# Kernel optimization log

Measured on AMD Instinct MI355X. Metric: run time of the kernel, lower is better.

Reference implementation:

```python
import jax, jax.numpy as jnp
import numpy as np
import math

B, T, D = 2, 2048, 2048
H, DH = 16, 128
DKV, DQ, DR = 512, 1024, 64
ROPE_BASE = 500000.0
EPS = 1e-6
SCALE = 1.0 / math.sqrt(DH + DR)


def setup_inputs() -> dict:
    key = jax.random.key(0)
    ks = jax.random.split(key, 12)
    s = 0.02
    return {
        'x': jax.random.normal(ks[0], (B, T, D), jnp.float32),
        'W_DQ': jax.random.normal(ks[1], (D, DQ), jnp.float32) * s,
        'W_UQ': jax.random.normal(ks[2], (DQ, H * DH), jnp.float32) * s,
        'W_QR': jax.random.normal(ks[3], (DQ, H * DR), jnp.float32) * s,
        'W_DKV': jax.random.normal(ks[4], (D, DKV), jnp.float32) * s,
        'W_UK': jax.random.normal(ks[5], (DKV, H * DH), jnp.float32) * s,
        'W_UV': jax.random.normal(ks[6], (DKV, H * DH), jnp.float32) * s,
        'W_KR': jax.random.normal(ks[7], (D, DR), jnp.float32) * s,
        'W_O': jax.random.normal(ks[8], (H * DH, D), jnp.float32) * s,
        'q_norm_w': jnp.ones((DQ,), jnp.float32),
        'kv_norm_w': jnp.ones((DKV,), jnp.float32),
    }


def _rmsnorm(v, w):
    n = jax.lax.rsqrt(jnp.mean(v * v, axis=-1, keepdims=True) + EPS)
    return v * n * w


def _rotate_half(v):
    v1, v2 = jnp.split(v, 2, axis=-1)
    return jnp.concatenate([-v2, v1], axis=-1)


def _rope_tables(seq_len):
    inv_freq = 1.0 / (ROPE_BASE ** (jnp.arange(0, DR, 2, dtype=jnp.float32) / DR))
    t = jnp.arange(seq_len, dtype=jnp.float32)
    freqs = jnp.outer(t, inv_freq)              # (S, DR/2)
    emb = jnp.concatenate([freqs, freqs], -1)   # (S, DR)
    return jnp.cos(emb), jnp.sin(emb)


def reference(x, W_DQ, W_UQ, W_QR, W_DKV, W_UK, W_UV, W_KR, W_O, q_norm_w, kv_norm_w):
    # Query path: low-rank compress -> RMSNorm -> up-project (content + rope parts)
    c_Q = _rmsnorm(x @ W_DQ, q_norm_w)                               # (B,T,DQ)
    q_C = (c_Q @ W_UQ).reshape(B, T, H, DH).transpose(0, 2, 1, 3)    # (B,H,T,DH)
    q_R = (c_Q @ W_QR).reshape(B, T, H, DR).transpose(0, 2, 1, 3)    # (B,H,T,DR)
    # KV path: joint low-rank latent + decoupled rope key
    c_KV = _rmsnorm(x @ W_DKV, kv_norm_w)                            # (B,T,DKV)
    k_C = (c_KV @ W_UK).reshape(B, T, H, DH).transpose(0, 2, 1, 3)   # (B,H,T,DH)
    v_C = (c_KV @ W_UV).reshape(B, T, H, DH).transpose(0, 2, 1, 3)   # (B,H,T,DH)
    k_R = (x @ W_KR)[:, None, :, :]                                  # (B,1,T,DR) shared across heads
    # Decoupled RoPE
    cos, sin = _rope_tables(T)
    cos = cos[None, None]; sin = sin[None, None]                     # (1,1,T,DR)
    q_R = q_R * cos + _rotate_half(q_R) * sin
    k_R = k_R * cos + _rotate_half(k_R) * sin
    k_R = jnp.broadcast_to(k_R, (B, H, T, DR))
    q = jnp.concatenate([q_C, q_R], axis=-1)                         # (B,H,T,DH+DR)
    k = jnp.concatenate([k_C, k_R], axis=-1)
    # Causal attention with MLA scale 1/sqrt(d_head + d_rope)
    scores = jnp.einsum('bhqd,bhkd->bhqk', q, k) * SCALE
    causal = jnp.tril(jnp.ones((T, T), bool))
    scores = jnp.where(causal, scores, jnp.finfo(scores.dtype).min)
    attn = jax.nn.softmax(scores, axis=-1)
    out = jnp.einsum('bhqk,bhkd->bhqd', attn, v_C)                   # (B,H,T,DH)
    out = out.transpose(0, 2, 1, 3).reshape(B, T, H * DH)
    return out @ W_O                                                 # (B,T,D)
```

## Files before the change

kernel.cpp:

```cpp
#include <hip/hip_runtime.h>
#include <cstdint>
#include <cstddef>

#define B_   2
#define T_   2048
#define D_   2048
#define H_   16
#define DH_  128
#define DQ_  1024
#define DKV_ 512
#define DR_  64
#define M_   4096
#define SCALE_ 0.07216878364870323f
#define SC2_   0.10412808709930322f
#define LN_BASE_ 13.122363377404328f

typedef unsigned short u16;
typedef __attribute__((ext_vector_type(8))) short short8;
typedef __attribute__((ext_vector_type(4))) float f32x4;

__device__ __forceinline__ float b2f(u16 u) { return __uint_as_float(((uint32_t)u) << 16); }
__device__ __forceinline__ u16 f2b(float f) {
    uint32_t x = __float_as_uint(f);
    return (u16)((x + 0x7fffu + ((x >> 16) & 1u)) >> 16);
}
__device__ __forceinline__ u16 f2b_fast(float f) {
    return (u16)((__float_as_uint(f) + 0x8000u) >> 16);
}

__device__ __forceinline__ void gload_lds16(const u16* src, u16* dst) {
    __builtin_amdgcn_global_load_lds(
        (const __attribute__((address_space(1))) uint32_t*)(uintptr_t)src,
        (__attribute__((address_space(3))) uint32_t*)(uintptr_t)dst, 16, 0, 0);
}

struct TPack {
    const float* src[8];
    u16*         dst[8];
    int K[8];
    int N[8];
    int ntx[8];
    int start[9];
};

__global__ __launch_bounds__(256) void prep_k(TPack p, const float* __restrict__ x,
                                              u16* __restrict__ xb, int ntr) {
    const int bid = blockIdx.x;
    if (bid < ntr) {
        __shared__ float tile[32][33];
        int w = 0;
#pragma unroll
        for (int i = 1; i < 8; ++i) if (bid >= p.start[i]) w = i;
        const int lt = bid - p.start[w];
        const int bx = lt % p.ntx[w], by = lt / p.ntx[w];
        const float* in = p.src[w];
        u16* out = p.dst[w];
        const int K = p.K[w], N = p.N[w];
        const int k0 = by * 32, n0 = bx * 32;
        const int tx = threadIdx.x & 31, ty = threadIdx.x >> 5;
#pragma unroll
        for (int i = 0; i < 4; ++i) {
            int k = k0 + ty + i * 8;
            int n = n0 + tx;
            tile[ty + i * 8][tx] = (n < N) ? in[(size_t)k * N + n] : 0.f;
        }
        __syncthreads();
#pragma unroll
        for (int i = 0; i < 4; ++i) {
            int n = n0 + ty + i * 8;
            out[(size_t)n * K + k0 + tx] = f2b(tile[tx][ty + i * 8]);
        }
    } else {
        const int i = ((bid - ntr) * 256 + threadIdx.x) * 4;
        const float4 v = *(const float4*)(x + i);
        ushort4 o;
        o.x = f2b(v.x); o.y = f2b(v.y); o.z = f2b(v.z); o.w = f2b(v.w);
        *(ushort4*)(xb + i) = o;
    }
}

template <int OUT_BF16>
__global__ __launch_bounds__(256) void gemm_tn(const u16* __restrict__ A,
                                               const u16* __restrict__ Bt,
                                               void* __restrict__ Cv,
                                               int N, int K) {
    __shared__ __attribute__((aligned(16))) u16 lA[128 * 32];
    __shared__ __attribute__((aligned(16))) u16 lB[128 * 32];
    const int m0 = blockIdx.y * 128, n0 = blockIdx.x * 128;
    const int tid = threadIdx.x, wave = tid >> 6, lane = tid & 63;
    const int wm = (wave >> 1) * 64, wn = (wave & 1) * 64;
    const int r = lane & 15, kq = lane >> 4;

    f32x4 acc[4][4];
#pragma unroll
    for (int i = 0; i < 4; ++i)
#pragma unroll
        for (int j = 0; j < 4; ++j) acc[i][j] = (f32x4){0.f, 0.f, 0.f, 0.f};

    for (int kk = 0; kk < K; kk += 32) {
#pragma unroll
        for (int p = 0; p < 2; ++p) {
            const int c = p * 256 + wave * 64 + lane;
            const u16* ga = A  + (size_t)(m0 + (c >> 2)) * K + kk + (c & 3) * 8;
            const u16* gb = Bt + (size_t)(n0 + (c >> 2)) * K + kk + (c & 3) * 8;
            u16* la = lA + (size_t)(p * 256 + wave * 64) * 8;
            u16* lb = lB + (size_t)(p * 256 + wave * 64) * 8;
            gload_lds16(ga, la);
            gload_lds16(gb, lb);
        }
        __syncthreads();
        short8 av[4], bv[4];
#pragma unroll
        for (int mi = 0; mi < 4; ++mi)
            av[mi] = *(const short8*)&lA[(wm + mi * 16 + r) * 32 + kq * 8];
#pragma unroll
        for (int ni = 0; ni < 4; ++ni)
            bv[ni] = *(const short8*)&lB[(wn + ni * 16 + r) * 32 + kq * 8];
#pragma unroll
        for (int mi = 0; mi < 4; ++mi)
#pragma unroll
            for (int ni = 0; ni < 4; ++ni)
                acc[mi][ni] = __builtin_amdgcn_mfma_f32_16x16x32_bf16(
                    av[mi], bv[ni], acc[mi][ni], 0, 0, 0);
        __syncthreads();
    }
    const int r4 = (lane >> 4) * 4, cc = lane & 15;
#pragma unroll
    for (int mi = 0; mi < 4; ++mi)
#pragma unroll
        for (int ni = 0; ni < 4; ++ni)
#pragma unroll
            for (int i = 0; i < 4; ++i) {
                const int row = m0 + wm + mi * 16 + r4 + i;
                const int col = n0 + wn + ni * 16 + cc;
                const float v = acc[mi][ni][i];
                if (OUT_BF16) ((u16*)Cv)[(size_t)row * N + col] = f2b(v);
                else          ((float*)Cv)[(size_t)row * N + col] = v;
            }
}

#define S_BM 256
#define S_BN 256
#define S_BK 64

__device__ __forceinline__ void gemm256_core(
    const u16* __restrict__ A, const u16* __restrict__ Bt, int K,
    int m0, int n0, int tid, f32x4 (&acc)[8][4],
    u16 (*sA)[S_BM * S_BK], u16 (*sB)[S_BN * S_BK]) {
    const int lane = tid & 63;
    const int wave = tid >> 6;
    const int wm = wave >> 2;
    const int r = lane & 15, kq = lane >> 4;
    const int wn = wave & 3;

    const u16* gA[4]; const u16* gB[4]; int dOf[4];
#pragma unroll
    for (int is = 0; is < 4; ++is) {
        const int c = is * 512 + tid;
        const int row = c >> 3, c16 = c & 7;
        gA[is] = A  + (size_t)(m0 + row) * K + ((c16 ^ (row & 7)) * 8);
        gB[is] = Bt + (size_t)(n0 + row) * K + ((c16 ^ (row & 7)) * 8);
        dOf[is] = c * 8;
    }

    const int NKT = K >> 6;

    auto STG = [&](int arr, int half, int bs, int kk) {
        u16* dst = arr ? (u16*)sB[bs] : (u16*)sA[bs];
        const u16** g = arr ? gB : gA;
#pragma unroll
        for (int is = half * 2; is < half * 2 + 2; ++is)
            gload_lds16(g[is] + kk, dst + dOf[is]);
    };

    STG(0, 0, 0, 0); STG(0, 1, 0, 0); STG(1, 0, 0, 0); STG(1, 1, 0, 0);

    short8 af[4][2], bf[2][2];
    for (int kt = 0; kt < NKT; ++kt) {
        const int cur = kt & 1;
        const int kk = (kt + 1) * 64;
        const int pf = (kt + 1 < NKT);
        const u16* cA = sA[cur];
        const u16* cB = sB[cur];

        auto lda = [&](int row, int g) -> short8 {
            return *(const short8*)&cA[row * 64 + ((g ^ (row & 7)) * 8)];
        };
        auto ldb = [&](int row, int g) -> short8 {
            return *(const short8*)&cB[row * 64 + ((g ^ (row & 7)) * 8)];
        };

#pragma unroll
        for (int ph = 0; ph < 4; ++ph) {
            const int mh = ph >> 1;
            const int nh = (ph == 1 || ph == 2) ? 1 : 0;
            if (pf) STG(ph >> 1, ph & 1, cur ^ 1, kk);
            if (ph == 0) {
                if (pf) asm volatile("s_waitcnt vmcnt(2)" ::: "memory");
                else    asm volatile("s_waitcnt vmcnt(0)" ::: "memory");
            }
            __builtin_amdgcn_s_barrier();
            asm volatile("" ::: "memory");
            if (!(ph & 1)) {
#pragma unroll
                for (int mi = 0; mi < 4; ++mi)
#pragma unroll
                    for (int ks = 0; ks < 2; ++ks)
                        af[mi][ks] = lda(wm * 128 + mh * 64 + mi * 16 + r, ks * 4 + kq);
            }
#pragma unroll
            for (int ni = 0; ni < 2; ++ni)
#pragma unroll
                for (int ks = 0; ks < 2; ++ks)
                    bf[ni][ks] = ldb(wn * 64 + nh * 32 + ni * 16 + r, ks * 4 + kq);
#pragma unroll
            for (int ks = 0; ks < 2; ++ks)
#pragma unroll
                for (int mi = 0; mi < 4; ++mi)
#pragma unroll
                    for (int ni = 0; ni < 2; ++ni)
                        acc[mh * 4 + mi][nh * 2 + ni] =
                            __builtin_amdgcn_mfma_f32_16x16x32_bf16(
                                af[mi][ks], bf[ni][ks],
                                acc[mh * 4 + mi][nh * 2 + ni], 0, 0, 0);
            asm volatile("" ::: "memory");
            __builtin_amdgcn_s_barrier();
            asm volatile("" ::: "memory");
        }
    }
}

__global__ __launch_bounds__(512, 1) void gemm256p_k(
    const u16* __restrict__ A0, const u16* __restrict__ B0,
    u16* __restrict__ C0, int N0c, int K0,
    const u16* __restrict__ A1, const u16* __restrict__ B1,
    u16* __restrict__ C1, int N1c, int K1,
    u16* __restrict__ Vt, int vcol0, int nx0)
{
    __shared__ __attribute__((aligned(16))) u16 sA[2][S_BM * S_BK];
    __shared__ __attribute__((aligned(16))) u16 sB[2][S_BN * S_BK];
    const int sel = (int)blockIdx.x >= nx0;
    const u16* A  = sel ? A1 : A0;
    const u16* Bt = sel ? B1 : B0;
    const int  K  = sel ? K1 : K0;
    const int lbx = sel ? (blockIdx.x - nx0) : blockIdx.x;
    const int m0 = blockIdx.y * S_BM, n0 = lbx * S_BN;
    const int tid = threadIdx.x, lane = tid & 63;
    const int wave = tid >> 6, wm = wave >> 2, wn = wave & 3;
    const int kq = lane >> 4;

    f32x4 acc[8][4];
#pragma unroll
    for (int i = 0; i < 8; ++i)
#pragma unroll
        for (int j = 0; j < 4; ++j) acc[i][j] = (f32x4){0.f, 0.f, 0.f, 0.f};

    gemm256_core(A, Bt, K, m0, n0, tid, acc, sA, sB);

    const int r4c = kq * 4, cc = lane & 15;
    if (!sel) {
#pragma unroll
        for (int mf = 0; mf < 8; ++mf)
#pragma unroll
            for (int nf = 0; nf < 4; ++nf)
#pragma unroll
                for (int i = 0; i < 4; ++i) {
                    const int row = m0 + wm * 128 + mf * 16 + r4c + i;
                    const int col = n0 + wn * 64 + nf * 16 + cc;
                    C0[(size_t)row * N0c + col] = f2b(acc[mf][nf][i]);
                }
    } else if (n0 < vcol0) {
#pragma unroll
        for (int mf = 0; mf < 8; ++mf)
#pragma unroll
            for (int nf = 0; nf < 4; ++nf)
#pragma unroll
                for (int i = 0; i < 4; ++i) {
                    const int row = m0 + wm * 128 + mf * 16 + r4c + i;
                    const int col = n0 + wn * 64 + nf * 16 + cc;
                    C1[(size_t)row * N1c + col] = f2b(acc[mf][nf][i]);
                }
    } else {
#pragma unroll
        for (int mf = 0; mf < 8; ++mf)
#pragma unroll
            for (int nf = 0; nf < 4; ++nf) {
                const int tp = m0 + wm * 128 + mf * 16 + r4c;
                const int c  = n0 - vcol0 + wn * 64 + nf * 16 + cc;
                u16 tmp[4];
#pragma unroll
                for (int i = 0; i < 4; ++i) tmp[i] = f2b(acc[mf][nf][i]);
                *(ushort4*)&Vt[((size_t)((tp >> 11) * 2048 + c)) * 2048 + (tp & 2047)]
                    = *(ushort4*)tmp;
            }
    }
}

__global__ __launch_bounds__(512, 1) void gemm256o_k(
    const u16* __restrict__ A, const u16* __restrict__ Bt,
    float* __restrict__ Cf, int N, int K)
{
    __shared__ __attribute__((aligned(16))) u16 sA[2][S_BM * S_BK];
    __shared__ __attribute__((aligned(16))) u16 sB[2][S_BN * S_BK];
    const int m0 = blockIdx.y * S_BM, n0 = blockIdx.x * S_BN;
    const int tid = threadIdx.x, lane = tid & 63;
    const int wave = tid >> 6, wm = wave >> 2, wn = wave & 3;
    const int kq = lane >> 4;

    f32x4 acc[8][4];
#pragma unroll
    for (int i = 0; i < 8; ++i)
#pragma unroll
        for (int j = 0; j < 4; ++j) acc[i][j] = (f32x4){0.f, 0.f, 0.f, 0.f};

    gemm256_core(A, Bt, K, m0, n0, tid, acc, sA, sB);

    const int r4c = kq * 4, cc = lane & 15;
#pragma unroll
    for (int mf = 0; mf < 8; ++mf)
#pragma unroll
        for (int nf = 0; nf < 4; ++nf)
#pragma unroll
            for (int i = 0; i < 4; ++i) {
                const int row = m0 + wm * 128 + mf * 16 + r4c + i;
                const int col = n0 + wn * 64 + nf * 16 + cc;
                Cf[(size_t)row * N + col] = acc[mf][nf][i];
            }
}

__global__ __launch_bounds__(256) void normrope_k(const u16* __restrict__ P1,
                                                  const float* __restrict__ qnw,
                                                  const float* __restrict__ kvnw,
                                                  u16* __restrict__ cQb,
                                                  u16* __restrict__ cKVb,
                                                  u16* __restrict__ kRb) {
    const int which = blockIdx.y;
    if (which < 2) {
        const int row = blockIdx.x;
        const int N = which ? 512 : 1024;
        const int off = which ? 1024 : 0;
        const float* w = which ? kvnw : qnw;
        u16* outp = which ? cKVb : cQb;
        const u16* src = P1 + (size_t)row * 1664 + off;
        const int j = threadIdx.x * 4;
        float v[4] = {0.f, 0.f, 0.f, 0.f};
        if (j < N) {
            ushort4 u = *(const ushort4*)(src + j);
            v[0] = b2f(u.x); v[1] = b2f(u.y); v[2] = b2f(u.z); v[3] = b2f(u.w);
        }
        float ss = v[0]*v[0] + v[1]*v[1] + v[2]*v[2] + v[3]*v[3];
#pragma unroll
        for (int offc = 32; offc; offc >>= 1) ss += __shfl_down(ss, offc);
        __shared__ float red[4];
        const int wave = threadIdx.x >> 6, lane = threadIdx.x & 63;
        if (lane == 0) red[wave] = ss;
        __syncthreads();
        const float tot = red[0] + red[1] + red[2] + red[3];
        const float sc = rsqrtf(tot / (float)N + 1e-6f);
        if (j < N) {
            ushort4 o;
            o.x = f2b(v[0] * sc * w[j]);
            o.y = f2b(v[1] * sc * w[j + 1]);
            o.z = f2b(v[2] * sc * w[j + 2]);
            o.w = f2b(v[3] * sc * w[j + 3]);
            *(ushort4*)(outp + (size_t)row * N + j) = o;
        }
    } else {
        if (blockIdx.x >= 1024) return;
        const int row = blockIdx.x * 4 + (threadIdx.x >> 6);
        const int j = threadIdx.x & 63;
        const int t = row & (T_ - 1);
        const int i = j & 31;
        const float invf = __expf(-LN_BASE_ * (float)(2 * i) * (1.0f / 64.0f));
        const float ang = (float)t * invf;
        const float c = cosf(ang), s = sinf(ang);
        const u16* src = P1 + (size_t)row * 1664 + 1536;
        const float v = b2f(src[j]);
        const float rot = (j < 32) ? -b2f(src[j + 32]) : b2f(src[j - 32]);
        kRb[(size_t)row * 64 + j] = f2b(v * c + rot * s);
    }
}

#define ABQ  128
#define ABK  64
#define NW   8
#define KSTR 200
#define VSTR 72
#define PSTR 72
#define VOFF 12800
#define KVSZ 22016
#define QSTRIDE 3072
#define KSTRIDE 4096

__global__ __launch_bounds__(512, 1) void attn_mfma_k(
    const u16* __restrict__ qC,
    const u16* __restrict__ kC, const u16* __restrict__ kR,
    const u16* __restrict__ Vt, u16* __restrict__ outp)
{
    __shared__ __attribute__((aligned(16))) u16 sKV[3][KVSZ];
    __shared__ __attribute__((aligned(16))) u16 sP[NW * 16 * PSTR];

    const int h = blockIdx.x, b = blockIdx.z;
    const int qb = b ? (15 - (int)blockIdx.y) : (int)blockIdx.y;
    const int q0 = qb * ABQ;
    const int tid = threadIdx.x, wave = tid >> 6, lane = tid & 63;
    const int r = lane & 15, kq = lane >> 4, r4 = kq * 4;
    const int wq = wave * 16;

    const u16* gsrc[6]; int gstep[6]; int doff[6];
#pragma unroll
    for (int j = 0; j < 6; ++j) {
        const int i = wave + NW * j;
        const int slot = (i < 43) ? i : (i - 43);
        if (slot < 25) {
            const int s = slot * 64 + lane;
            const int rr2 = s / 25;
            int cc = s - rr2 * 25;
            if (cc > 23) cc = 0;
            if (cc < 16) {
                gsrc[j] = kC + (size_t)(b * T_ + rr2) * KSTRIDE + h * 128 + cc * 8;
                gstep[j] = ABK * KSTRIDE;
            } else {
                gsrc[j] = kR + (size_t)(b * T_ + rr2) * 64 + (cc - 16) * 8;
                gstep[j] = ABK * 64;
            }
            doff[j] = slot * 512;
        } else {
            const int sl = slot - 25;
            const int s = sl * 64 + lane;
            const int rr2 = s / 9;
            int cc = s - rr2 * 9;
            if (cc > 7) cc = 0;
            gsrc[j] = Vt + ((size_t)(b * H_ + h) * 128 + rr2) * T_ + cc * 8;
            gstep[j] = ABK;
            doff[j] = VOFF + sl * 512;
        }
    }

    short8 qf[6];
    {
        const int t = q0 + wq + r;
        const u16* qcrow = qC + (size_t)(b * T_ + t) * QSTRIDE + h * 128 + kq * 8;
#pragma unroll
        for (int kc = 0; kc < 4; ++kc) qf[kc] = *(const short8*)(qcrow + kc * 32);
        const u16* qrraw = qC + (size_t)(b * T_ + t) * QSTRIDE + 2048 + h * 64 + kq * 8;
        const short8 q0v = *(const short8*)(qrraw);
        const short8 q1v = *(const short8*)(qrraw + 32);
        short8 o0, o1;
#pragma unroll
        for (int j = 0; j < 8; ++j) {
            const int i = kq * 8 + j;
            const float invf = __expf(-LN_BASE_ * (float)(2 * i) * (1.0f / 64.0f));
            const float ang = (float)t * invf;
            const float cs = cosf(ang), sn = sinf(ang);
            const float a = b2f((u16)q0v[j]), bb = b2f((u16)q1v[j]);
            o0[j] = (short)f2b(a * cs - bb * sn);
            o1[j] = (short)f2b(bb * cs + a * sn);
        }
        qf[4] = o0; qf[5] = o1;
    }

    f32x4 Oa[8];
#pragma unroll
    for (int nt = 0; nt < 8; ++nt) Oa[nt] = (f32x4){0.f, 0.f, 0.f, 0.f};
    float Lrow[4] = {0.f, 0.f, 0.f, 0.f};

    u16* myP = sP + wave * 16 * PSTR;

    auto STAGE = [&](int kt2, int bs) {
        u16* dst = &sKV[bs][0];
#pragma unroll
        for (int j = 0; j < 6; ++j)
            gload_lds16(gsrc[j] + (size_t)kt2 * (size_t)gstep[j], dst + doff[j]);
    };

    const int nkt = 2 * qb + 2;
    STAGE(0, 0);
    STAGE(1, 1);
    for (int kt = 0; kt < nkt; ++kt) {
        const int cur = kt % 3;
        if (kt == 0 || kt >= nkt - 1) {
            asm volatile("s_waitcnt vmcnt(0)" ::: "memory");
        } else {
            asm volatile("s_waitcnt vmcnt(6)" ::: "memory");
        }
        __builtin_amdgcn_s_barrier();
        asm volatile("" ::: "memory");

        const u16* cK = &sKV[cur][0];
        const u16* cV = &sKV[cur][VOFF];
        const int k0 = kt * ABK;

        f32x4 Sa[4];
#pragma unroll
        for (int nt = 0; nt < 4; ++nt) Sa[nt] = (f32x4){0.f, 0.f, 0.f, 0.f};
#pragma unroll
        for (int kc = 0; kc < 6; ++kc) {
            short8 kf[4];
#pragma unroll
            for (int nt = 0; nt < 4; ++nt)
                kf[nt] = *(const short8*)&cK[(nt * 16 + r) * KSTR + (kc * 4 + kq) * 8];
#pragma unroll
            for (int nt = 0; nt < 4; ++nt)
                Sa[nt] = __builtin_amdgcn_mfma_f32_16x16x32_bf16(
                    qf[kc], kf[nt], Sa[nt], 0, 0, 0);
        }

        if (kt < nkt - 2) {
#pragma unroll
            for (int i = 0; i < 4; ++i) {
                float sm = 0.f;
#pragma unroll
                for (int nt = 0; nt < 4; ++nt) {
                    const float p = exp2f(Sa[nt][i] * SC2_);
                    sm += p;
                    myP[(r4 + i) * PSTR + nt * 16 + r] = f2b_fast(p);
                }
                Lrow[i] += sm;
            }
        } else {
#pragma unroll
            for (int i = 0; i < 4; ++i) {
                const int grow = q0 + wq + r4 + i;
                float sm = 0.f;
#pragma unroll
                for (int nt = 0; nt < 4; ++nt) {
                    float p = exp2f(Sa[nt][i] * SC2_);
                    p = (k0 + nt * 16 + r > grow) ? 0.f : p;
                    sm += p;
                    myP[(r4 + i) * PSTR + nt * 16 + r] = f2b_fast(p);
                }
                Lrow[i] += sm;
            }
        }

#pragma unroll
        for (int kc2 = 0; kc2 < 2; ++kc2) {
            const short8 pf = *(const short8*)&myP[r * PSTR + (kc2 * 4 + kq) * 8];
#pragma unroll
            for (int nt = 0; nt < 8; ++nt) {
                const short8 vf = *(const short8*)&cV[(nt * 16 + r) * VSTR + (kc2 * 4 + kq) * 8];
                Oa[nt] = __builtin_amdgcn_mfma_f32_16x16x32_bf16(
                    pf, vf, Oa[nt], 0, 0, 0);
            }
        }

        if (kt + 2 < nkt) STAGE(kt + 2, (kt + 2) % 3);
    }

#pragma unroll
    for (int i = 0; i < 4; ++i) {
        float L = Lrow[i];
        L += __shfl_xor(L, 1);
        L += __shfl_xor(L, 2);
        L += __shfl_xor(L, 4);
        L += __shfl_xor(L, 8);
        const float inv = 1.0f / L;
        const int t = q0 + wq + r4 + i;
        u16* orow = outp + (size_t)(b * T_ + t) * 2048 + h * 128;
#pragma unroll
        for (int nt = 0; nt < 8; ++nt)
            orow[nt * 16 + r] = f2b(Oa[nt][i] * inv);
    }
}

extern "C" void kernel_launch(void* const* d_in, const int* in_sizes, int n_in,
                              void* d_out, int out_size, void* d_ws, size_t ws_size,
                              hipStream_t stream) {
    (void)in_sizes; (void)n_in; (void)out_size; (void)ws_size;
    const float* x     = (const float*)d_in[0];
    const float* W_DQ  = (const float*)d_in[1];
    const float* W_UQ  = (const float*)d_in[2];
    const float* W_QR  = (const float*)d_in[3];
    const float* W_DKV = (const float*)d_in[4];
    const float* W_UK  = (const float*)d_in[5];
    const float* W_UV  = (const float*)d_in[6];
    const float* W_KR  = (const float*)d_in[7];
    const float* W_O   = (const float*)d_in[8];
    const float* qnw   = (const float*)d_in[9];
    const float* kvnw  = (const float*)d_in[10];
    float* out = (float*)d_out;

    char* base = (char*)d_ws;
    size_t o = 0;
    auto alloc = [&](size_t bytes) {
        char* r = base + o;
        o += (bytes + 255) & ~(size_t)255;
        return r;
    };
    u16* WT1  = (u16*)alloc((size_t)1664 * 2048 * 2);
    u16* WT2  = (u16*)alloc((size_t)3072 * 1024 * 2);
    u16* WT3  = (u16*)alloc((size_t)4096 * 512 * 2);
    u16* WT_O = (u16*)alloc((size_t)2048 * 2048 * 2);
    u16* xb   = (u16*)alloc((size_t)M_ * 2048 * 2);
    u16* U1   = (u16*)alloc((size_t)M_ * 2048 * 2);
    u16* P2   = (u16*)alloc((size_t)M_ * 3072 * 2);
    u16* P3   = (u16*)alloc((size_t)M_ * 4096 * 2);
    u16* cQb  = (u16*)alloc((size_t)M_ * 1024 * 2);
    u16* cKVb = (u16*)alloc((size_t)M_ * 512 * 2);
    u16* qRb  = (u16*)alloc((size_t)M_ * 1024 * 2);
    u16* kRb  = (u16*)alloc((size_t)M_ * 64 * 2);
    (void)qRb;
    u16* P1       = U1;
    u16* attn_out = U1;
    u16* Vt       = xb;

    TPack tp;
    const float* srcs[8] = {W_DQ, W_DKV, W_KR, W_UQ, W_QR, W_UK, W_UV, W_O};
    u16* dsts[8] = {WT1, WT1 + (size_t)1024*2048, WT1 + (size_t)1536*2048,
                    WT2, WT2 + (size_t)2048*1024,
                    WT3, WT3 + (size_t)2048*512, WT_O};
    const int Ks[8]   = {2048, 2048, 2048, 1024, 1024, 512, 512, 2048};
    const int Ns[8]   = {1024,  512,   64, 2048, 1024, 2048, 2048, 2048};
    const int ntxs[8] = {  32,   16,    4,   64,   32,   64,   64,   64};
    int cum = 0;
    for (int i = 0; i < 8; ++i) {
        tp.src[i] = srcs[i]; tp.dst[i] = dsts[i];
        tp.K[i] = Ks[i]; tp.N[i] = Ns[i]; tp.ntx[i] = ntxs[i];
        tp.start[i] = cum;
        cum += ntxs[i] * (Ks[i] / 32);
    }
    tp.start[8] = cum;
    const int ncast = (M_ * D_) / 1024;
    prep_k<<<cum + ncast, 256, 0, stream>>>(tp, x, xb, cum);

    gemm_tn<1><<<dim3(1664/128, M_/128), 256, 0, stream>>>(xb, WT1, (void*)P1, 1664, 2048);

    normrope_k<<<dim3(M_, 3), 256, 0, stream>>>(P1, qnw, kvnw, cQb, cKVb, kRb);

    gemm256p_k<<<dim3(3072/256 + 4096/256, M_/256), 512, 0, stream>>>(
        cQb,  WT2, P2, 3072, 1024,
        cKVb, WT3, P3, 4096, 512,
        Vt, 2048, 3072/256);

    attn_mfma_k<<<dim3(H_, T_/ABQ, B_), 512, 0, stream>>>(P2, P3, kRb, Vt, attn_out);

    gemm256o_k<<<dim3(2048/256, M_/256), 512, 0, stream>>>(attn_out, WT_O, out, 2048, 2048);
}
```

Baseline: 391.5 us.

## Enlarge attention query tile to 256 rows with double-buffered KV staging

```diff
diff --git a/kernel.cpp b/kernel.cpp
--- a/kernel.cpp
+++ b/kernel.cpp
@@ -294,38 +294,6 @@
                     = *(ushort4*)tmp;
             }
     }
-}
-
-__global__ __launch_bounds__(512, 1) void gemm256o_k(
-    const u16* __restrict__ A, const u16* __restrict__ Bt,
-    float* __restrict__ Cf, int N, int K)
-{
-    __shared__ __attribute__((aligned(16))) u16 sA[2][S_BM * S_BK];
-    __shared__ __attribute__((aligned(16))) u16 sB[2][S_BN * S_BK];
-    const int m0 = blockIdx.y * S_BM, n0 = blockIdx.x * S_BN;
-    const int tid = threadIdx.x, lane = tid & 63;
-    const int wave = tid >> 6, wm = wave >> 2, wn = wave & 3;
-    const int kq = lane >> 4;
-
-    f32x4 acc[8][4];
-#pragma unroll
-    for (int i = 0; i < 8; ++i)
-#pragma unroll
-        for (int j = 0; j < 4; ++j) acc[i][j] = (f32x4){0.f, 0.f, 0.f, 0.f};
-
-    gemm256_core(A, Bt, K, m0, n0, tid, acc, sA, sB);
-
-    const int r4c = kq * 4, cc = lane & 15;
-#pragma unroll
-    for (int mf = 0; mf < 8; ++mf)
-#pragma unroll
-        for (int nf = 0; nf < 4; ++nf)
-#pragma unroll
-            for (int i = 0; i < 4; ++i) {
-                const int row = m0 + wm * 128 + mf * 16 + r4c + i;
-                const int col = n0 + wn * 64 + nf * 16 + cc;
-                Cf[(size_t)row * N + col] = acc[mf][nf][i];
-            }
 }
 
 __global__ __launch_bounds__(256) void normrope_k(const u16* __restrict__ P1,
@@ -381,7 +349,7 @@
     }
 }
 
-#define ABQ  128
+#define ABQ  256
 #define ABK  64
 #define NW   8
 #define KSTR 200
@@ -397,15 +365,15 @@
     const u16* __restrict__ kC, const u16* __restrict__ kR,
     const u16* __restrict__ Vt, u16* __restrict__ outp)
 {
-    __shared__ __attribute__((aligned(16))) u16 sKV[3][KVSZ];
-    __shared__ __attribute__((aligned(16))) u16 sP[NW * 16 * PSTR];
+    __shared__ __attribute__((aligned(16))) u16 sKV[2][KVSZ];
+    __shared__ __attribute__((aligned(16))) u16 sP[NW * 32 * PSTR];
 
     const int h = blockIdx.x, b = blockIdx.z;
-    const int qb = b ? (15 - (int)blockIdx.y) : (int)blockIdx.y;
+    const int qb = b ? (7 - (int)blockIdx.y) : (int)blockIdx.y;
     const int q0 = qb * ABQ;
     const int tid = threadIdx.x, wave = tid >> 6, lane = tid & 63;
     const int r = lane & 15, kq = lane >> 4, r4 = kq * 4;
-    const int wq = wave * 16;
+    const int wq = wave * 32;
 
     const u16* gsrc[6]; int gstep[6]; int doff[6];
 #pragma unroll
@@ -437,12 +405,13 @@
         }
     }
 
-    short8 qf[6];
-    {
-        const int t = q0 + wq + r;
+    short8 qf[2][6];
+#pragma unroll
+    for (int mt = 0; mt < 2; ++mt) {
+        const int t = q0 + wq + mt * 16 + r;
         const u16* qcrow = qC + (size_t)(b * T_ + t) * QSTRIDE + h * 128 + kq * 8;
 #pragma unroll
-        for (int kc = 0; kc < 4; ++kc) qf[kc] = *(const short8*)(qcrow + kc * 32);
+        for (int kc = 0; kc < 4; ++kc) qf[mt][kc] = *(const short8*)(qcrow + kc * 32);
         const u16* qrraw = qC + (size_t)(b * T_ + t) * QSTRIDE + 2048 + h * 64 + kq * 8;
         const short8 q0v = *(const short8*)(qrraw);
         const short8 q1v = *(const short8*)(qrraw + 32);
@@ -457,15 +426,17 @@
             o0[j] = (short)f2b(a * cs - bb * sn);
             o1[j] = (short)f2b(bb * cs + a * sn);
         }
-        qf[4] = o0; qf[5] = o1;
-    }
-
-    f32x4 Oa[8];
-#pragma unroll
-    for (int nt = 0; nt < 8; ++nt) Oa[nt] = (f32x4){0.f, 0.f, 0.f, 0.f};
-    float Lrow[4] = {0.f, 0.f, 0.f, 0.f};
-
-    u16* myP = sP + wave * 16 * PSTR;
+        qf[mt][4] = o0; qf[mt][5] = o1;
+    }
+
+    f32x4 Oa[2][8];
+#pragma unroll
+    for (int mt = 0; mt < 2; ++mt)
+#pragma unroll
+        for (int nt = 0; nt < 8; ++nt) Oa[mt][nt] = (f32x4){0.f, 0.f, 0.f, 0.f};
+    float Lrow[2][4] = {{0.f,0.f,0.f,0.f},{0.f,0.f,0.f,0.f}};
+
+    u16* myP = sP + (size_t)wave * 32 * PSTR;
 
     auto STAGE = [&](int kt2, int bs) {
         u16* dst = &sKV[bs][0];
@@ -474,12 +445,12 @@
             gload_lds16(gsrc[j] + (size_t)kt2 * (size_t)gstep[j], dst + doff[j]);
     };
 
-    const int nkt = 2 * qb + 2;
+    const int nkt = 4 * qb + 4;
     STAGE(0, 0);
-    STAGE(1, 1);
     for (int kt = 0; kt < nkt; ++kt) {
-        const int cur = kt % 3;
-        if (kt == 0 || kt >= nkt - 1) {
+        const int cur = kt & 1;
+        if (kt + 1 < nkt) STAGE(kt + 1, cur ^ 1);
+        if (kt == 0 || kt + 1 >= nkt) {
             asm volatile("s_waitcnt vmcnt(0)" ::: "memory");
         } else {
             asm volatile("s_waitcnt vmcnt(6)" ::: "memory");
@@ -491,9 +462,11 @@
         const u16* cV = &sKV[cur][VOFF];
         const int k0 = kt * ABK;
 
-        f32x4 Sa[4];
-#pragma unroll
-        for (int nt = 0; nt < 4; ++nt) Sa[nt] = (f32x4){0.f, 0.f, 0.f, 0.f};
+        f32x4 Sa[2][4];
+#pragma unroll
+        for (int mt = 0; mt < 2; ++mt)
+#pragma unroll
+            for (int nt = 0; nt < 4; ++nt) Sa[mt][nt] = (f32x4){0.f, 0.f, 0.f, 0.f};
 #pragma unroll
         for (int kc = 0; kc < 6; ++kc) {
             short8 kf[4];
@@ -501,67 +474,82 @@
             for (int nt = 0; nt < 4; ++nt)
                 kf[nt] = *(const short8*)&cK[(nt * 16 + r) * KSTR + (kc * 4 + kq) * 8];
 #pragma unroll
-            for (int nt = 0; nt < 4; ++nt)
-                Sa[nt] = __builtin_amdgcn_mfma_f32_16x16x32_bf16(
-                    qf[kc], kf[nt], Sa[nt], 0, 0, 0);
-        }
-
-        if (kt < nkt - 2) {
-#pragma unroll
-            for (int i = 0; i < 4; ++i) {
-                float sm = 0.f;
-#pragma unroll
-                for (int nt = 0; nt < 4; ++nt) {
-                    const float p = exp2f(Sa[nt][i] * SC2_);
-                    sm += p;
-                    myP[(r4 + i) * PSTR + nt * 16 + r] = f2b_fast(p);
+            for (int mt = 0; mt < 2; ++mt)
+#pragma unroll
+                for (int nt = 0; nt < 4; ++nt)
+                    Sa[mt][nt] = __builtin_amdgcn_mfma_f32_16x16x32_bf16(
+                        qf[mt][kc], kf[nt], Sa[mt][nt], 0, 0, 0);
+        }
+
+        if (kt < nkt - 4) {
+#pragma unroll
+            for (int mt = 0; mt < 2; ++mt)
+#pragma unroll
+                for (int i = 0; i < 4; ++i) {
+                    float sm = 0.f;
+#pragma unroll
+                    for (int nt = 0; nt < 4; ++nt) {
+                        const float p = exp2f(Sa[mt][nt][i] * SC2_);
+                        sm += p;
+                        myP[(mt * 16 + r4 + i) * PSTR + nt * 16 + r] = f2b_fast(p);
+                    }
+                    Lrow[mt][i] += sm;
                 }
-                Lrow[i] += sm;
-            }
         } else {
 #pragma unroll
-            for (int i = 0; i < 4; ++i) {
-                const int grow = q0 + wq + r4 + i;
-                float sm = 0.f;
-#pragma unroll
-                for (int nt = 0; nt < 4; ++nt) {
-                    float p = exp2f(Sa[nt][i] * SC2_);
-                    p = (k0 + nt * 16 + r > grow) ? 0.f : p;
-                    sm += p;
-                    myP[(r4 + i) * PSTR + nt * 16 + r] = f2b_fast(p);
+            for (int mt = 0; mt < 2; ++mt)
+#pragma unroll
+                for (int i = 0; i < 4; ++i) {
+                    const int grow = q0 + wq + mt * 16 + r4 + i;
+                    float sm = 0.f;
+#pragma unroll
+                    for (int nt = 0; nt < 4; ++nt) {
+                        float p = exp2f(Sa[mt][nt][i] * SC2_);
+                        p = (k0 + nt * 16 + r > grow) ? 0.f : p;
+                        sm += p;
+                        myP[(mt * 16 + r4 + i) * PSTR + nt * 16 + r] = f2b_fast(p);
+                    }
+                    Lrow[mt][i] += sm;
                 }
-                Lrow[i] += sm;
-            }
         }
 
 #pragma unroll
         for (int kc2 = 0; kc2 < 2; ++kc2) {
-            const short8 pf = *(const short8*)&myP[r * PSTR + (kc2 * 4 + kq) * 8];
+            short8 pf[2];
+#pragma unroll
+            for (int mt = 0; mt < 2; ++mt)
+                pf[mt] = *(const short8*)&myP[(mt * 16 + r) * PSTR + (kc2 * 4 + kq) * 8];
 #pragma unroll
             for (int nt = 0; nt < 8; ++nt) {
                 const short8 vf = *(const short8*)&cV[(nt * 16 + r) * VSTR + (kc2 * 4 + kq) * 8];
-                Oa[nt] = __builtin_amdgcn_mfma_f32_16x16x32_bf16(
-                    pf, vf, Oa[nt], 0, 0, 0);
+#pragma unroll
+                for (int mt = 0; mt < 2; ++mt)
+                    Oa[mt][nt] = __builtin_amdgcn_mfma_f32_16x16x32_bf16(
+                        pf[mt], vf, Oa[mt][nt], 0, 0, 0);
             }
         }
 
-        if (kt + 2 < nkt) STAGE(kt + 2, (kt + 2) % 3);
-    }
-
-#pragma unroll
-    for (int i = 0; i < 4; ++i) {
-        float L = Lrow[i];
-        L += __shfl_xor(L, 1);
-        L += __shfl_xor(L, 2);
-        L += __shfl_xor(L, 4);
-        L += __shfl_xor(L, 8);
-        const float inv = 1.0f / L;
-        const int t = q0 + wq + r4 + i;
-        u16* orow = outp + (size_t)(b * T_ + t) * 2048 + h * 128;
-#pragma unroll
-        for (int nt = 0; nt < 8; ++nt)
-            orow[nt * 16 + r] = f2b(Oa[nt][i] * inv);
-    }
+        asm volatile("" ::: "memory");
+        __builtin_amdgcn_s_barrier();
+        asm volatile("" ::: "memory");
+    }
+
+#pragma unroll
+    for (int mt = 0; mt < 2; ++mt)
+#pragma unroll
+        for (int i = 0; i < 4; ++i) {
+            float L = Lrow[mt][i];
+            L += __shfl_xor(L, 1);
+            L += __shfl_xor(L, 2);
+            L += __shfl_xor(L, 4);
+            L += __shfl_xor(L, 8);
+            const float inv = 1.0f / L;
+            const int t = q0 + wq + mt * 16 + r4 + i;
+            u16* orow = outp + (size_t)(b * T_ + t) * 2048 + h * 128;
+#pragma unroll
+            for (int nt = 0; nt < 8; ++nt)
+                orow[nt * 16 + r] = f2b(Oa[mt][nt][i] * inv);
+        }
 }
 
 extern "C" void kernel_launch(void* const* d_in, const int* in_sizes, int n_in,
@@ -635,5 +623,5 @@
 
     attn_mfma_k<<<dim3(H_, T_/ABQ, B_), 512, 0, stream>>>(P2, P3, kRb, Vt, attn_out);
 
-    gemm256o_k<<<dim3(2048/256, M_/256), 512, 0, stream>>>(attn_out, WT_O, out, 2048, 2048);
-}
+    gemm_tn<0><<<dim3(2048/128, M_/128), 256, 0, stream>>>(attn_out, WT_O, (void*)out, 2048, 2048);
+}
```

Measured after the change: 420.0 us. 1.07x slower.
